# Optimization experiments

Hardware: AMD Instinct MI355X
Metric: run time of the kernel (lower is better)

The kernel has to match this reference:

```python
import jax, jax.numpy as jnp
import numpy as np

NEG = -1e30          # stand-in for -inf that is safe in fp arithmetic
EPS = 1e-7           # keras.backend.epsilon()

B, T, C, L = 64, 1024, 128, 256
BLANK = C - 1        # keras ctc_batch_cost uses last class as blank


def setup_inputs() -> dict:
    key = jax.random.key(0)
    k1, k2, k3 = jax.random.split(key, 3)
    # ctc_batch_cost expects softmax probabilities, not logits
    y_pred = jax.nn.softmax(jax.random.normal(k1, (B, T, C), dtype=jnp.float32), axis=-1)
    y_true = jax.random.randint(k2, (B, L), 0, C - 1).astype(jnp.int32)  # labels exclude blank
    input_length = jnp.full((B, 1), T, dtype=jnp.int32)
    label_length = jax.random.randint(k3, (B, 1), 1, L + 1).astype(jnp.int32)
    return {"y_true": y_true, "y_pred": y_pred,
            "input_length": input_length, "label_length": label_length}


def _logsumexp3(a, b, c):
    m = jnp.maximum(a, jnp.maximum(b, c))
    return m + jnp.log(jnp.exp(a - m) + jnp.exp(b - m) + jnp.exp(c - m))


def _ctc_loss(y_pred, y_true, input_length, label_length):
    log_probs = jnp.log(y_pred + EPS)                       # [B,T,C]
    S = 2 * L + 1
    # extended label sequence: blank, l0, blank, l1, ..., blank
    ext = jnp.full((B, S), BLANK, dtype=jnp.int32).at[:, 1::2].set(y_true)
    lab_len = label_length[:, 0]                            # [B]
    s_idx = jnp.arange(S)
    valid_s = s_idx[None, :] < (2 * lab_len + 1)[:, None]   # [B,S]
    # skip (s-2 -> s) allowed only for non-blank, non-repeated symbols
    skip_ok = jnp.concatenate(
        [jnp.zeros((B, 2), bool),
         (ext[:, 2:] != BLANK) & (ext[:, 2:] != ext[:, :-2])], axis=1)
    # gather per-extended-position log-probs: [B,T,S]
    lp_ext = jnp.take_along_axis(log_probs, jnp.broadcast_to(ext[:, None, :], (B, T, S)), axis=2)

    alpha0 = jnp.full((B, S), NEG, dtype=log_probs.dtype)
    alpha0 = alpha0.at[:, 0].set(lp_ext[:, 0, 0])
    alpha0 = alpha0.at[:, 1].set(jnp.where(lab_len > 0, lp_ext[:, 0, 1], NEG))
    alpha0 = jnp.where(valid_s, alpha0, NEG)

    def step(alpha, inp):
        lp_t, t = inp                                       # lp_t: [B,S]
        shift1 = jnp.pad(alpha[:, :-1], ((0, 0), (1, 0)), constant_values=NEG)
        shift2 = jnp.pad(alpha[:, :-2], ((0, 0), (2, 0)), constant_values=NEG)
        shift2 = jnp.where(skip_ok, shift2, NEG)
        new = _logsumexp3(alpha, shift1, shift2) + lp_t
        new = jnp.where(valid_s, new, NEG)
        # freeze alpha past each sample's input_length
        new = jnp.where(t < input_length, new, alpha)
        return new, None

    lp_tmaj = jnp.swapaxes(lp_ext, 0, 1)                    # [T,B,S]
    alpha, _ = jax.lax.scan(step, alpha0, (lp_tmaj[1:], jnp.arange(1, T)))

    end_blank = jnp.take_along_axis(alpha, (2 * lab_len)[:, None], axis=1)[:, 0]
    end_label = jnp.take_along_axis(alpha, jnp.maximum(2 * lab_len - 1, 0)[:, None], axis=1)[:, 0]
    end_label = jnp.where(lab_len > 0, end_label, NEG)
    loss = -jnp.logaddexp(end_blank, end_label)             # [B]
    return loss[:, None]                                    # (batch, 1) like ctc_batch_cost


def reference(y_true, y_pred, input_length, label_length):
    return _ctc_loss(y_pred, y_true, input_length, label_length)
```

## Files before the change

kernel.cpp:

```cpp
#include <hip/hip_runtime.h>


#define Bc 64
#define Tc 1024
#define Cc 128
#define Lc 256
#define Sc 513
#define BLANKc 127
#define CHUNK 32
#define NW 4
#define PADS 64
#define WSSTRIDE 1028

constexpr float EPSF = 1e-7f;

#define DPPMAXI(x, ctrl) max(x, __builtin_amdgcn_update_dpp( \
    0, x, ctrl, 0xf, 0xf, true))

__device__ __forceinline__ double dpp_wave_shr1_f64(double x) {
    union { double d; int i[2]; } u, r;
    u.d = x;
    r.i[0] = __builtin_amdgcn_update_dpp(0, u.i[0], 0x138, 0xf, 0xf, true);
    r.i[1] = __builtin_amdgcn_update_dpp(0, u.i[1], 0x138, 0xf, 0xf, true);
    return r.d;
}
__device__ __forceinline__ double dpp_wave_shl1_f64(double x) {
    union { double d; int i[2]; } u, r;
    u.d = x;
    r.i[0] = __builtin_amdgcn_update_dpp(0, u.i[0], 0x130, 0xf, 0xf, true);
    r.i[1] = __builtin_amdgcn_update_dpp(0, u.i[1], 0x130, 0xf, 0xf, true);
    return r.d;
}

__global__ __launch_bounds__(256) void ctc_fb_kernel(
    const int* __restrict__ y_true,
    const float* __restrict__ y_pred,
    const int* __restrict__ label_length,
    double* __restrict__ ws)
{
    const int bb = blockIdx.x;
    const int b = bb >> 1;
    const bool isF = !(bb & 1);
    const int tid = (int)threadIdx.x;
    const int wl = tid >> 6;
    const int lane = tid & 63;

    __shared__ float bufs[3][CHUNK * Cc];
    __shared__ double ash[Sc];
    __shared__ int em[NW];

    const int lab_len = label_length[b];
    const float* yp = y_pred + (size_t)b * Tc * Cc;
    const int* lab = y_true + b * Lc;
    double* wsb = ws + (size_t)b * WSSTRIDE;

    const int start = isF ? ((wl == 0) ? 0 : (128 * wl - PADS)) : (128 * wl);
    const int own_s = 128 * wl;
    const int own_e = (wl == NW - 1) ? Sc : (128 * (wl + 1));
    const int s0 = start + 4 * lane;

    const int li0 = s0 >> 1;
    const int li0c = min(li0, Lc - 1);
    const int li1c = min(li0 + 1, Lc - 1);
    const int li2c = min(li0 + 2, Lc - 1);
    const int ca = lab[li0c], cb = lab[li1c], cc = lab[li2c];
    const double sm_a = (li0 > 0 && ca != BLANKc && ca != lab[li0c - 1]) ? 1.0 : 0.0;
    const double sm_b = (cb != BLANKc && cb != ca) ? 1.0 : 0.0;
    const double sm_c = (cc != BLANKc && cc != cb) ? 1.0 : 0.0;

    const int S2 = 2 * lab_len + 1;
    const bool ow0 = (s0     >= own_s) && (s0     < own_e);
    const bool ow1 = (s0 + 1 >= own_s) && (s0 + 1 < own_e);
    const bool ow2 = (s0 + 2 >= own_s) && (s0 + 2 < own_e);
    const bool ow3 = (s0 + 3 >= own_s) && (s0 + 3 < own_e);
    const int om0 = (ow0 && s0     < S2) ? -1 : 0;
    const int om1 = (ow1 && s0 + 1 < S2) ? -1 : 0;
    const int om2 = (ow2 && s0 + 2 < S2) ? -1 : 0;
    const int om3 = (ow3 && s0 + 3 < S2) ? -1 : 0;

    auto stage = [&](int c, float* dst) {
        const float* g = yp + (size_t)c * (CHUNK * Cc) + lane * 4;
        #pragma unroll
        for (int q = 0; q < 4; ++q) {
            const int i = wl * 4 + q;
            __builtin_amdgcn_global_load_lds(
                (const __attribute__((address_space(1))) void*)(g + i * 256),
                (__attribute__((address_space(3))) void*)(dst + i * 256),
                16, 0, 0);
        }
    };

    if (isF) {
        double a0 = 0, a1 = 0, a2 = 0, a3 = 0, n3 = 0;
        int tote = 0;
        double Eb, Ea, Ec;
        double Ob, Oa, Oc;
        float sl[4][6];

        auto gpair = [&](const float* rowp, float* s) {
            s[0] = rowp[BLANKc]; s[1] = rowp[BLANKc + Cc];
            s[2] = rowp[ca];     s[3] = rowp[ca + Cc];
            s[4] = rowp[cb];     s[5] = rowp[cb + Cc];
        };
        auto expandE = [&](const float* s) {
            Eb = (double)(s[0] + EPSF); Ea = (double)(s[2] + EPSF);
            Ec = (double)(s[4] + EPSF);
        };
        auto expandO = [&](const float* s) {
            Ob = (double)(s[1] + EPSF); Oa = (double)(s[3] + EPSF);
            Oc = (double)(s[5] + EPSF);
        };
        auto stepE = [&]() {
            const double t3 = __fma_rn(sm_b, a1, a3 + a2);
            const double t2 = a2 + a1;
            const double t1 = __fma_rn(sm_a, n3, a1 + a0);
            const double t0 = a0 + n3;
            a3 = t3 * Ec;
            n3 = dpp_wave_shr1_f64(a3);
            a2 = t2 * Eb; a1 = t1 * Ea; a0 = t0 * Eb;
        };
        auto stepO = [&]() {
            const double t3 = __fma_rn(sm_b, a1, a3 + a2);
            const double t2 = a2 + a1;
            const double t1 = __fma_rn(sm_a, n3, a1 + a0);
            const double t0 = a0 + n3;
            a3 = t3 * Oc;
            n3 = dpp_wave_shr1_f64(a3);
            a2 = t2 * Ob; a1 = t1 * Oa; a0 = t0 * Ob;
        };
        auto syncex = [&](int sk) {
            int e =        om0 & (__double2hiint(a0) >> 20);
            e = max(e, om1 & (__double2hiint(a1) >> 20));
            e = max(e, om2 & (__double2hiint(a2) >> 20));
            e = max(e, om3 & (__double2hiint(a3) >> 20));
            e = DPPMAXI(e, 0x111); e = DPPMAXI(e, 0x112);
            e = DPPMAXI(e, 0x114); e = DPPMAXI(e, 0x118);
            e = DPPMAXI(e, 0x142); e = DPPMAXI(e, 0x143);
            if (lane == 63) em[wl] = e;
            if (ow0) ash[s0]     = a0;
            if (ow1) ash[s0 + 1] = a1;
            if (ow2) ash[s0 + 2] = a2;
            if (ow3) ash[s0 + 3] = a3;
            __syncthreads();
            const int eg = max(max(em[0], em[1]), max(em[2], em[3]));
            const int sexp = min(max(2046 - eg, 1), 2045);
            const double sc = __hiloint2double(sexp << 20, 0);
            tote += 1023 - sexp;
            if (wl > 0 && lane < (PADS / 4)) {
                a0 = ash[s0];     a1 = ash[s0 + 1];
                a2 = ash[s0 + 2]; a3 = ash[s0 + 3];
            }
            a0 *= sc; a1 *= sc; a2 *= sc; a3 *= sc;
            n3 = dpp_wave_shr1_f64(a3);
            __syncthreads();
            if (sk <= 15) stage(sk, bufs[sk % 3]);
        };

        stage(0, bufs[0]); stage(1, bufs[1]); stage(2, bufs[2]);
        __syncthreads();

        if (wl == 0 && lane == 0) {
            a0 = (double)(bufs[0][BLANKc] + EPSF);
            if (lab_len > 0) a1 = (double)(bufs[0][ca] + EPSF);
        }
        gpair(bufs[0] + 2 * Cc, sl[1]);
        gpair(bufs[0] + 4 * Cc, sl[2]);
        gpair(bufs[0] + 6 * Cc, sl[3]);
        {
            const float* r1 = bufs[0] + 1 * Cc;
            Ob = (double)(r1[BLANKc] + EPSF);
            Oa = (double)(r1[ca] + EPSF);
            Oc = (double)(r1[cb] + EPSF);
        }
        expandE(sl[1]);

        stepO();
        expandO(sl[1]);

        {
            const float* rb  = bufs[0];
            const float* rbn = bufs[1];
            #pragma unroll
            for (int qi = 1; qi < 16; ++qi) {
                const int rr = 2 * qi;
                const float* nxt = (rr + 6 < CHUNK) ? (rb + (rr + 6) * Cc)
                                                    : (rbn + (rr + 6 - CHUNK) * Cc);
                gpair(nxt, sl[(qi + 3) & 3]);
                stepE();
                expandE(sl[(qi + 1) & 3]);
                stepO();
                expandO(sl[(qi + 1) & 3]);
            }
        }
        for (int k = 1; k < 16; ++k) {
            syncex(k + 2);
            const float* rb  = bufs[k % 3];
            const float* rbn = bufs[(k + 1) % 3];
            #pragma unroll
            for (int qi = 0; qi < 16; ++qi) {
                const int rr = 2 * qi;
                const float* nxt = (rr + 6 < CHUNK) ? (rb + (rr + 6) * Cc)
                                                    : (rbn + (rr + 6 - CHUNK) * Cc);
                gpair(nxt, sl[(qi + 3) & 3]);
                stepE();
                expandE(sl[(qi + 1) & 3]);
                stepO();
                expandO(sl[(qi + 1) & 3]);
            }
        }
        if (ow0) wsb[s0]     = a0;
        if (ow1) wsb[s0 + 1] = a1;
        if (ow2) wsb[s0 + 2] = a2;
        if (ow3) wsb[s0 + 3] = a3;
        if (tid == 0) wsb[513] = (double)tote;
    } else {
        double b0 = 0, b1 = 0, b2 = 0, b3 = 0, n0 = 0, n1 = 0;
        int tote = 0;
        double Eb, Ea, Ec, Ed;
        double Ob, Oa, Oc, Od;
        float sl[4][8];

        auto gpair = [&](const float* rowp, float* s) {
            s[0] = rowp[BLANKc]; s[1] = rowp[BLANKc + Cc];
            s[2] = rowp[ca];     s[3] = rowp[ca + Cc];
            s[4] = rowp[cb];     s[5] = rowp[cb + Cc];
            s[6] = rowp[cc];     s[7] = rowp[cc + Cc];
        };
        auto expandE = [&](const float* s) {
            Eb = (double)(s[0] + EPSF); Ea = (double)(s[2] + EPSF);
            Ec = (double)(s[4] + EPSF); Ed = (double)(s[6] + EPSF);
        };
        auto expandO = [&](const float* s) {
            Ob = (double)(s[1] + EPSF); Oa = (double)(s[3] + EPSF);
            Oc = (double)(s[5] + EPSF); Od = (double)(s[7] + EPSF);
        };
        auto stepBE = [&]() {
            const double x1 = Ea * b1, x2 = Eb * b2, x3 = Ec * b3, z = Ed * n1;
            const double r0 = __fma_rn(Eb, b0, x1);
            const double r1 = __fma_rn(sm_b, x3, x1 + x2);
            const double r2 = x2 + x3;
            const double r3 = __fma_rn(sm_c, z, __fma_rn(Eb, n0, x3));
            b0 = r0; b1 = r1; b2 = r2; b3 = r3;
            n0 = dpp_wave_shl1_f64(b0);
            n1 = dpp_wave_shl1_f64(b1);
        };
        auto stepBO = [&]() {
            const double x1 = Oa * b1, x2 = Ob * b2, x3 = Oc * b3, z = Od * n1;
            const double r0 = __fma_rn(Ob, b0, x1);
            const double r1 = __fma_rn(sm_b, x3, x1 + x2);
            const double r2 = x2 + x3;
            const double r3 = __fma_rn(sm_c, z, __fma_rn(Ob, n0, x3));
            b0 = r0; b1 = r1; b2 = r2; b3 = r3;
            n0 = dpp_wave_shl1_f64(b0);
            n1 = dpp_wave_shl1_f64(b1);
        };
        auto syncex = [&](int sk) {
            int e =        om0 & (__double2hiint(b0) >> 20);
            e = max(e, om1 & (__double2hiint(b1) >> 20));
            e = max(e, om2 & (__double2hiint(b2) >> 20));
            e = max(e, om3 & (__double2hiint(b3) >> 20));
            e = DPPMAXI(e, 0x111); e = DPPMAXI(e, 0x112);
            e = DPPMAXI(e, 0x114); e = DPPMAXI(e, 0x118);
            e = DPPMAXI(e, 0x142); e = DPPMAXI(e, 0x143);
            if (lane == 63) em[wl] = e;
            if (ow0) ash[s0]     = b0;
            if (ow1) ash[s0 + 1] = b1;
            if (ow2) ash[s0 + 2] = b2;
            if (ow3) ash[s0 + 3] = b3;
            __syncthreads();
            const int eg = max(max(em[0], em[1]), max(em[2], em[3]));
            const int sexp = min(max(2046 - eg, 1), 2045);
            const double sc = __hiloint2double(sexp << 20, 0);
            tote += 1023 - sexp;
            if (s0     >= own_e) b0 = (s0     < Sc) ? ash[s0]     : 0.0;
            if (s0 + 1 >= own_e) b1 = (s0 + 1 < Sc) ? ash[s0 + 1] : 0.0;
            if (s0 + 2 >= own_e) b2 = (s0 + 2 < Sc) ? ash[s0 + 2] : 0.0;
            if (s0 + 3 >= own_e) b3 = (s0 + 3 < Sc) ? ash[s0 + 3] : 0.0;
            b0 *= sc; b1 *= sc; b2 *= sc; b3 *= sc;
            n0 = dpp_wave_shl1_f64(b0);
            n1 = dpp_wave_shl1_f64(b1);
            __syncthreads();
            if (sk >= 16) stage(sk, bufs[(31 - sk) % 3]);
        };

        stage(31, bufs[0]); stage(30, bufs[1]); stage(29, bufs[2]);
        __syncthreads();

        {
            const int e0 = 2 * lab_len;
            const int e1 = (lab_len > 0) ? (2 * lab_len - 1) : e0;
            b0 = (s0     == e0 || s0     == e1) ? 1.0 : 0.0;
            b1 = (s0 + 1 == e0 || s0 + 1 == e1) ? 1.0 : 0.0;
            b2 = (s0 + 2 == e0 || s0 + 2 == e1) ? 1.0 : 0.0;
            b3 = (s0 + 3 == e0 || s0 + 3 == e1) ? 1.0 : 0.0;
            n0 = dpp_wave_shl1_f64(b0);
            n1 = dpp_wave_shl1_f64(b1);
        }
        gpair(bufs[0] + 30 * Cc, sl[3]);
        gpair(bufs[0] + 28 * Cc, sl[2]);
        gpair(bufs[0] + 26 * Cc, sl[1]);
        expandO(sl[3]);
        expandE(sl[3]);

        {
            const float* rb  = bufs[0];
            const float* rbn = bufs[1];
            #pragma unroll
            for (int j = 0; j < 16; ++j) {
                const int q = 15 - j;
                const int rr = 2 * q;
                const float* nxt = (rr - 6 >= 0) ? (rb + (rr - 6) * Cc)
                                                 : (rbn + (rr - 6 + CHUNK) * Cc);
                gpair(nxt, sl[(q + 1) & 3]);
                stepBO();
                expandO(sl[(q - 1) & 3]);
                stepBE();
                expandE(sl[(q - 1) & 3]);
            }
        }
        for (int c = 30; c >= 16; --c) {
            syncex(c - 2);
            const float* rb  = bufs[(31 - c) % 3];
            const float* rbn = bufs[(32 - c) % 3];
            #pragma unroll
            for (int j = 0; j < 16; ++j) {
                const int q = 15 - j;
                const int rr = 2 * q;
                const float* nxt = (rr - 6 >= 0) ? (rb + (rr - 6) * Cc)
                                                 : (rbn + (rr - 6 + CHUNK) * Cc);
                gpair(nxt, sl[(q + 1) & 3]);
                stepBO();
                expandO(sl[(q - 1) & 3]);
                stepBE();
                expandE(sl[(q - 1) & 3]);
            }
        }
        if (ow0) wsb[514 + s0]     = b0;
        if (ow1) wsb[514 + s0 + 1] = b1;
        if (ow2) wsb[514 + s0 + 2] = b2;
        if (ow3) wsb[514 + s0 + 3] = b3;
        if (tid == 0) wsb[1027] = (double)tote;
    }
}

__global__ __launch_bounds__(64) void ctc_combine(
    const int* __restrict__ label_length,
    const double* __restrict__ ws,
    float* __restrict__ out)
{
    const int b = blockIdx.x;
    const int lane = (int)threadIdx.x;
    const int lab_len = label_length[b];
    const int S2 = 2 * lab_len + 1;
    const double* wf = ws + (size_t)b * WSSTRIDE;
    const double* wb = wf + 514;

    int eP = 0;
    for (int s = lane; s < S2; s += 64) {
        const int ea = (__double2hiint(wf[s]) >> 20) & 0x7ff;
        const int eb = (__double2hiint(wb[s]) >> 20) & 0x7ff;
        if (ea && eb) eP = max(eP, ea + eb);
    }
    #pragma unroll
    for (int m = 1; m < 64; m <<= 1) eP = max(eP, __shfl_xor(eP, m));
    const int sh = 2046 - eP;
    int k1 = sh / 2;
    int k2 = sh - k1;
    k1 = min(max(k1, -1022), 1023);
    k2 = min(max(k2, -1022), 1023);
    const double scA = __hiloint2double((1023 + k1) << 20, 0);
    const double scB = __hiloint2double((1023 + k2) << 20, 0);
    double dot = 0.0;
    for (int s = lane; s < S2; s += 64)
        dot += (wf[s] * scA) * (wb[s] * scB);
    #pragma unroll
    for (int m = 1; m < 64; m <<= 1) dot += __shfl_xor(dot, m);
    if (lane == 0) {
        const double lt = wf[513] + wb[513] - (double)k1 - (double)k2;
        out[b] = (float)(-(log(dot) + lt * 0.6931471805599453));
    }
}

extern "C" void kernel_launch(void* const* d_in, const int* in_sizes, int n_in,
                              void* d_out, int out_size, void* d_ws, size_t ws_size,
                              hipStream_t stream) {
    const int*   y_true       = (const int*)d_in[0];
    const float* y_pred       = (const float*)d_in[1];
    const int*   label_length = (const int*)d_in[3];
    float* out = (float*)d_out;
    double* ws = (double*)d_ws;

    ctc_fb_kernel<<<2 * Bc, NW * 64, 0, stream>>>(y_true, y_pred,
                                                  label_length, ws);
    ctc_combine<<<Bc, 64, 0, stream>>>(label_length, ws, out);
}
```

Measured before the change: 117.2 us.

## Split CTC forward/backward across 8 waves with 2 states per lane

Each block goes from 4 waves holding 4 extended-label states per lane to 8 waves holding 2 states per lane. Ownership ranges and the 64-position forward halo are redefined so each wave computes 128 positions and owns 64. This shortens the serial dependent FP64 work per time step in each lane. In exchange, every chunk sync barrier and exponent max-reduction now spans 8 waves, more redundant halo work is done, and the staging loads are spread over more waves.

```diff
diff --git a/kernel.cpp b/kernel.cpp
--- a/kernel.cpp
+++ b/kernel.cpp
@@ -8,8 +8,7 @@
 #define Sc 513
 #define BLANKc 127
 #define CHUNK 32
-#define NW 4
-#define PADS 64
+#define NW 8
 #define WSSTRIDE 1028
 
 constexpr float EPSF = 1e-7f;
@@ -32,7 +31,7 @@
     return r.d;
 }
 
-__global__ __launch_bounds__(256) void ctc_fb_kernel(
+__global__ __launch_bounds__(512) void ctc_fb_kernel(
     const int* __restrict__ y_true,
     const float* __restrict__ y_pred,
     const int* __restrict__ label_length,
@@ -54,35 +53,30 @@
     const int* lab = y_true + b * Lc;
     double* wsb = ws + (size_t)b * WSSTRIDE;
 
-    const int start = isF ? ((wl == 0) ? 0 : (128 * wl - PADS)) : (128 * wl);
-    const int own_s = 128 * wl;
-    const int own_e = (wl == NW - 1) ? Sc : (128 * (wl + 1));
-    const int s0 = start + 4 * lane;
+    const int start = 64 * wl;
+    const int s0 = start + 2 * lane;
+    const int own_s = isF ? ((wl == 0) ? 0 : (start + 64)) : start;
+    const int own_e = isF ? min(start + 128, Sc)
+                          : ((wl == NW - 1) ? Sc : (start + 64));
 
     const int li0 = s0 >> 1;
     const int li0c = min(li0, Lc - 1);
     const int li1c = min(li0 + 1, Lc - 1);
-    const int li2c = min(li0 + 2, Lc - 1);
-    const int ca = lab[li0c], cb = lab[li1c], cc = lab[li2c];
+    const int ca = lab[li0c], cb = lab[li1c];
     const double sm_a = (li0 > 0 && ca != BLANKc && ca != lab[li0c - 1]) ? 1.0 : 0.0;
     const double sm_b = (cb != BLANKc && cb != ca) ? 1.0 : 0.0;
-    const double sm_c = (cc != BLANKc && cc != cb) ? 1.0 : 0.0;
 
     const int S2 = 2 * lab_len + 1;
     const bool ow0 = (s0     >= own_s) && (s0     < own_e);
     const bool ow1 = (s0 + 1 >= own_s) && (s0 + 1 < own_e);
-    const bool ow2 = (s0 + 2 >= own_s) && (s0 + 2 < own_e);
-    const bool ow3 = (s0 + 3 >= own_s) && (s0 + 3 < own_e);
     const int om0 = (ow0 && s0     < S2) ? -1 : 0;
     const int om1 = (ow1 && s0 + 1 < S2) ? -1 : 0;
-    const int om2 = (ow2 && s0 + 2 < S2) ? -1 : 0;
-    const int om3 = (ow3 && s0 + 3 < S2) ? -1 : 0;
 
     auto stage = [&](int c, float* dst) {
         const float* g = yp + (size_t)c * (CHUNK * Cc) + lane * 4;
         #pragma unroll
-        for (int q = 0; q < 4; ++q) {
-            const int i = wl * 4 + q;
+        for (int q = 0; q < 2; ++q) {
+            const int i = wl * 2 + q;
             __builtin_amdgcn_global_load_lds(
                 (const __attribute__((address_space(1))) void*)(g + i * 256),
                 (__attribute__((address_space(3))) void*)(dst + i * 256),
@@ -91,67 +85,57 @@
     };
 
     if (isF) {
-        double a0 = 0, a1 = 0, a2 = 0, a3 = 0, n3 = 0;
+        double a0 = 0, a1 = 0, n1 = 0;
         int tote = 0;
-        double Eb, Ea, Ec;
-        double Ob, Oa, Oc;
-        float sl[4][6];
+        double Eb, Ea;
+        double Ob, Oa;
+        float sl[4][4];
 
         auto gpair = [&](const float* rowp, float* s) {
             s[0] = rowp[BLANKc]; s[1] = rowp[BLANKc + Cc];
             s[2] = rowp[ca];     s[3] = rowp[ca + Cc];
-            s[4] = rowp[cb];     s[5] = rowp[cb + Cc];
         };
         auto expandE = [&](const float* s) {
             Eb = (double)(s[0] + EPSF); Ea = (double)(s[2] + EPSF);
-            Ec = (double)(s[4] + EPSF);
         };
         auto expandO = [&](const float* s) {
             Ob = (double)(s[1] + EPSF); Oa = (double)(s[3] + EPSF);
-            Oc = (double)(s[5] + EPSF);
         };
         auto stepE = [&]() {
-            const double t3 = __fma_rn(sm_b, a1, a3 + a2);
-            const double t2 = a2 + a1;
-            const double t1 = __fma_rn(sm_a, n3, a1 + a0);
-            const double t0 = a0 + n3;
-            a3 = t3 * Ec;
-            n3 = dpp_wave_shr1_f64(a3);
-            a2 = t2 * Eb; a1 = t1 * Ea; a0 = t0 * Eb;
+            const double t1 = __fma_rn(sm_a, n1, a1 + a0);
+            const double t0 = a0 + n1;
+            a1 = t1 * Ea;
+            n1 = dpp_wave_shr1_f64(a1);
+            a0 = t0 * Eb;
         };
         auto stepO = [&]() {
-            const double t3 = __fma_rn(sm_b, a1, a3 + a2);
-            const double t2 = a2 + a1;
-            const double t1 = __fma_rn(sm_a, n3, a1 + a0);
-            const double t0 = a0 + n3;
-            a3 = t3 * Oc;
-            n3 = dpp_wave_shr1_f64(a3);
-            a2 = t2 * Ob; a1 = t1 * Oa; a0 = t0 * Ob;
+            const double t1 = __fma_rn(sm_a, n1, a1 + a0);
+            const double t0 = a0 + n1;
+            a1 = t1 * Oa;
+            n1 = dpp_wave_shr1_f64(a1);
+            a0 = t0 * Ob;
         };
         auto syncex = [&](int sk) {
             int e =        om0 & (__double2hiint(a0) >> 20);
             e = max(e, om1 & (__double2hiint(a1) >> 20));
-            e = max(e, om2 & (__double2hiint(a2) >> 20));
-            e = max(e, om3 & (__double2hiint(a3) >> 20));
             e = DPPMAXI(e, 0x111); e = DPPMAXI(e, 0x112);
             e = DPPMAXI(e, 0x114); e = DPPMAXI(e, 0x118);
             e = DPPMAXI(e, 0x142); e = DPPMAXI(e, 0x143);
             if (lane == 63) em[wl] = e;
             if (ow0) ash[s0]     = a0;
             if (ow1) ash[s0 + 1] = a1;
-            if (ow2) ash[s0 + 2] = a2;
-            if (ow3) ash[s0 + 3] = a3;
             __syncthreads();
-            const int eg = max(max(em[0], em[1]), max(em[2], em[3]));
+            int eg = em[0];
+            #pragma unroll
+            for (int w = 1; w < NW; ++w) eg = max(eg, em[w]);
             const int sexp = min(max(2046 - eg, 1), 2045);
             const double sc = __hiloint2double(sexp << 20, 0);
             tote += 1023 - sexp;
-            if (wl > 0 && lane < (PADS / 4)) {
-                a0 = ash[s0];     a1 = ash[s0 + 1];
-                a2 = ash[s0 + 2]; a3 = ash[s0 + 3];
-            }
-            a0 *= sc; a1 *= sc; a2 *= sc; a3 *= sc;
-            n3 = dpp_wave_shr1_f64(a3);
+            if (wl > 0 && lane < 32) {
+                a0 = ash[s0]; a1 = ash[s0 + 1];
+            }
+            a0 *= sc; a1 *= sc;
+            n1 = dpp_wave_shr1_f64(a1);
             __syncthreads();
             if (sk <= 15) stage(sk, bufs[sk % 3]);
         };
@@ -170,7 +154,6 @@
             const float* r1 = bufs[0] + 1 * Cc;
             Ob = (double)(r1[BLANKc] + EPSF);
             Oa = (double)(r1[ca] + EPSF);
-            Oc = (double)(r1[cb] + EPSF);
         }
         expandE(sl[1]);
 
@@ -210,73 +193,62 @@
         }
         if (ow0) wsb[s0]     = a0;
         if (ow1) wsb[s0 + 1] = a1;
-        if (ow2) wsb[s0 + 2] = a2;
-        if (ow3) wsb[s0 + 3] = a3;
         if (tid == 0) wsb[513] = (double)tote;
     } else {
-        double b0 = 0, b1 = 0, b2 = 0, b3 = 0, n0 = 0, n1 = 0;
+        double b0 = 0, b1 = 0, n0 = 0, n1 = 0;
         int tote = 0;
-        double Eb, Ea, Ec, Ed;
-        double Ob, Oa, Oc, Od;
-        float sl[4][8];
+        double Eb, Ea, Ec;
+        double Ob, Oa, Oc;
+        float sl[4][6];
 
         auto gpair = [&](const float* rowp, float* s) {
             s[0] = rowp[BLANKc]; s[1] = rowp[BLANKc + Cc];
             s[2] = rowp[ca];     s[3] = rowp[ca + Cc];
             s[4] = rowp[cb];     s[5] = rowp[cb + Cc];
-            s[6] = rowp[cc];     s[7] = rowp[cc + Cc];
         };
         auto expandE = [&](const float* s) {
             Eb = (double)(s[0] + EPSF); Ea = (double)(s[2] + EPSF);
-            Ec = (double)(s[4] + EPSF); Ed = (double)(s[6] + EPSF);
+            Ec = (double)(s[4] + EPSF);
         };
         auto expandO = [&](const float* s) {
             Ob = (double)(s[1] + EPSF); Oa = (double)(s[3] + EPSF);
-            Oc = (double)(s[5] + EPSF); Od = (double)(s[7] + EPSF);
+            Oc = (double)(s[5] + EPSF);
         };
         auto stepBE = [&]() {
-            const double x1 = Ea * b1, x2 = Eb * b2, x3 = Ec * b3, z = Ed * n1;
+            const double x1 = Ea * b1, x2 = Eb * n0, x3 = Ec * n1;
             const double r0 = __fma_rn(Eb, b0, x1);
             const double r1 = __fma_rn(sm_b, x3, x1 + x2);
-            const double r2 = x2 + x3;
-            const double r3 = __fma_rn(sm_c, z, __fma_rn(Eb, n0, x3));
-            b0 = r0; b1 = r1; b2 = r2; b3 = r3;
+            b0 = r0; b1 = r1;
             n0 = dpp_wave_shl1_f64(b0);
             n1 = dpp_wave_shl1_f64(b1);
         };
         auto stepBO = [&]() {
-            const double x1 = Oa * b1, x2 = Ob * b2, x3 = Oc * b3, z = Od * n1;
+            const double x1 = Oa * b1, x2 = Ob * n0, x3 = Oc * n1;
             const double r0 = __fma_rn(Ob, b0, x1);
             const double r1 = __fma_rn(sm_b, x3, x1 + x2);
-            const double r2 = x2 + x3;
-            const double r3 = __fma_rn(sm_c, z, __fma_rn(Ob, n0, x3));
-            b0 = r0; b1 = r1; b2 = r2; b3 = r3;
+            b0 = r0; b1 = r1;
             n0 = dpp_wave_shl1_f64(b0);
             n1 = dpp_wave_shl1_f64(b1);
         };
         auto syncex = [&](int sk) {
             int e =        om0 & (__double2hiint(b0) >> 20);
             e = max(e, om1 & (__double2hiint(b1) >> 20));
-            e = max(e, om2 & (__double2hiint(b2) >> 20));
-            e = max(e, om3 & (__double2hiint(b3) >> 20));
             e = DPPMAXI(e, 0x111); e = DPPMAXI(e, 0x112);
             e = DPPMAXI(e, 0x114); e = DPPMAXI(e, 0x118);
             e = DPPMAXI(e, 0x142); e = DPPMAXI(e, 0x143);
             if (lane == 63) em[wl] = e;
             if (ow0) ash[s0]     = b0;
             if (ow1) ash[s0 + 1] = b1;
-            if (ow2) ash[s0 + 2] = b2;
-            if (ow3) ash[s0 + 3] = b3;
             __syncthreads();
-            const int eg = max(max(em[0], em[1]), max(em[2], em[3]));
+            int eg = em[0];
+            #pragma unroll
+            for (int w = 1; w < NW; ++w) eg = max(eg, em[w]);
             const int sexp = min(max(2046 - eg, 1), 2045);
             const double sc = __hiloint2double(sexp << 20, 0);
             tote += 1023 - sexp;
             if (s0     >= own_e) b0 = (s0     < Sc) ? ash[s0]     : 0.0;
             if (s0 + 1 >= own_e) b1 = (s0 + 1 < Sc) ? ash[s0 + 1] : 0.0;
-            if (s0 + 2 >= own_e) b2 = (s0 + 2 < Sc) ? ash[s0 + 2] : 0.0;
-            if (s0 + 3 >= own_e) b3 = (s0 + 3 < Sc) ? ash[s0 + 3] : 0.0;
-            b0 *= sc; b1 *= sc; b2 *= sc; b3 *= sc;
+            b0 *= sc; b1 *= sc;
             n0 = dpp_wave_shl1_f64(b0);
             n1 = dpp_wave_shl1_f64(b1);
             __syncthreads();
@@ -291,8 +263,6 @@
             const int e1 = (lab_len > 0) ? (2 * lab_len - 1) : e0;
             b0 = (s0     == e0 || s0     == e1) ? 1.0 : 0.0;
             b1 = (s0 + 1 == e0 || s0 + 1 == e1) ? 1.0 : 0.0;
-            b2 = (s0 + 2 == e0 || s0 + 2 == e1) ? 1.0 : 0.0;
-            b3 = (s0 + 3 == e0 || s0 + 3 == e1) ? 1.0 : 0.0;
             n0 = dpp_wave_shl1_f64(b0);
             n1 = dpp_wave_shl1_f64(b1);
         }
@@ -337,8 +307,6 @@
         }
         if (ow0) wsb[514 + s0]     = b0;
         if (ow1) wsb[514 + s0 + 1] = b1;
-        if (ow2) wsb[514 + s0 + 2] = b2;
-        if (ow3) wsb[514 + s0 + 3] = b3;
         if (tid == 0) wsb[1027] = (double)tote;
     }
 }
```

New measurement: 117.7 us. No clear change (+0.4%).

## Bulk-load per-chunk probability columns into registers, fetch blank column from global

Applied to the files above, without the earlier changes.

Replaces the rolling 4-slot software pipeline of per-row LDS reads with a bulk load of all 32 rows of the needed columns into register arrays at the start of each chunk. The blank column is read straight from global memory rather than LDS, and the backward pass's fourth class column is obtained by a DPP lane shift of the neighbour's value instead of a separate LDS read. Launch bounds are set to one block per CU so the larger register arrays fit. The change cuts LDS traffic and address arithmetic inside the recurrence, but it adds register pressure and puts global-memory latency at the start of each chunk.

```diff
diff --git a/kernel.cpp b/kernel.cpp
--- a/kernel.cpp
+++ b/kernel.cpp
@@ -31,8 +31,14 @@
     r.i[1] = __builtin_amdgcn_update_dpp(0, u.i[1], 0x130, 0xf, 0xf, true);
     return r.d;
 }
-
-__global__ __launch_bounds__(256) void ctc_fb_kernel(
+__device__ __forceinline__ float dpp_wave_shl1_f32(float x) {
+    union { float f; int i; } u, r;
+    u.f = x;
+    r.i = __builtin_amdgcn_update_dpp(0, u.i, 0x130, 0xf, 0xf, true);
+    return r.f;
+}
+
+__global__ __launch_bounds__(256, 1) void ctc_fb_kernel(
     const int* __restrict__ y_true,
     const float* __restrict__ y_pred,
     const int* __restrict__ label_length,
@@ -90,26 +96,25 @@
         }
     };
 
+    float cB[CHUNK];
+    float cA[CHUNK];
+    float cC[CHUNK];
+
+    auto loadcols = [&](int c, const float* rb) {
+        const float* gB = yp + (size_t)c * (CHUNK * Cc) + BLANKc;
+        #pragma unroll
+        for (int t = 0; t < CHUNK; ++t) {
+            cA[t] = rb[t * Cc + ca];
+            cC[t] = rb[t * Cc + cb];
+            cB[t] = gB[t * Cc];
+        }
+    };
+
     if (isF) {
         double a0 = 0, a1 = 0, a2 = 0, a3 = 0, n3 = 0;
         int tote = 0;
-        double Eb, Ea, Ec;
-        double Ob, Oa, Oc;
-        float sl[4][6];
-
-        auto gpair = [&](const float* rowp, float* s) {
-            s[0] = rowp[BLANKc]; s[1] = rowp[BLANKc + Cc];
-            s[2] = rowp[ca];     s[3] = rowp[ca + Cc];
-            s[4] = rowp[cb];     s[5] = rowp[cb + Cc];
-        };
-        auto expandE = [&](const float* s) {
-            Eb = (double)(s[0] + EPSF); Ea = (double)(s[2] + EPSF);
-            Ec = (double)(s[4] + EPSF);
-        };
-        auto expandO = [&](const float* s) {
-            Ob = (double)(s[1] + EPSF); Oa = (double)(s[3] + EPSF);
-            Oc = (double)(s[5] + EPSF);
-        };
+        double Eb, Ea, Ec, Ob, Oa, Oc;
+
         auto stepE = [&]() {
             const double t3 = __fma_rn(sm_b, a1, a3 + a2);
             const double t2 = a2 + a1;
@@ -127,6 +132,16 @@
             a3 = t3 * Oc;
             n3 = dpp_wave_shr1_f64(a3);
             a2 = t2 * Ob; a1 = t1 * Oa; a0 = t0 * Ob;
+        };
+        auto dopair = [&](int r) {
+            Eb = (double)(cB[r] + EPSF);
+            Ea = (double)(cA[r] + EPSF);
+            Ec = (double)(cC[r] + EPSF);
+            stepE();
+            Ob = (double)(cB[r + 1] + EPSF);
+            Oa = (double)(cA[r + 1] + EPSF);
+            Oc = (double)(cC[r + 1] + EPSF);
+            stepO();
         };
         auto syncex = [&](int sk) {
             int e =        om0 & (__double2hiint(a0) >> 20);
@@ -159,54 +174,23 @@
         stage(0, bufs[0]); stage(1, bufs[1]); stage(2, bufs[2]);
         __syncthreads();
 
+        loadcols(0, bufs[0]);
         if (wl == 0 && lane == 0) {
-            a0 = (double)(bufs[0][BLANKc] + EPSF);
-            if (lab_len > 0) a1 = (double)(bufs[0][ca] + EPSF);
-        }
-        gpair(bufs[0] + 2 * Cc, sl[1]);
-        gpair(bufs[0] + 4 * Cc, sl[2]);
-        gpair(bufs[0] + 6 * Cc, sl[3]);
-        {
-            const float* r1 = bufs[0] + 1 * Cc;
-            Ob = (double)(r1[BLANKc] + EPSF);
-            Oa = (double)(r1[ca] + EPSF);
-            Oc = (double)(r1[cb] + EPSF);
-        }
-        expandE(sl[1]);
-
+            a0 = (double)(cB[0] + EPSF);
+            if (lab_len > 0) a1 = (double)(cA[0] + EPSF);
+        }
+        Ob = (double)(cB[1] + EPSF);
+        Oa = (double)(cA[1] + EPSF);
+        Oc = (double)(cC[1] + EPSF);
         stepO();
-        expandO(sl[1]);
-
-        {
-            const float* rb  = bufs[0];
-            const float* rbn = bufs[1];
-            #pragma unroll
-            for (int qi = 1; qi < 16; ++qi) {
-                const int rr = 2 * qi;
-                const float* nxt = (rr + 6 < CHUNK) ? (rb + (rr + 6) * Cc)
-                                                    : (rbn + (rr + 6 - CHUNK) * Cc);
-                gpair(nxt, sl[(qi + 3) & 3]);
-                stepE();
-                expandE(sl[(qi + 1) & 3]);
-                stepO();
-                expandO(sl[(qi + 1) & 3]);
-            }
-        }
+        #pragma unroll
+        for (int p = 1; p < 16; ++p) dopair(2 * p);
+
         for (int k = 1; k < 16; ++k) {
             syncex(k + 2);
-            const float* rb  = bufs[k % 3];
-            const float* rbn = bufs[(k + 1) % 3];
+            loadcols(k, bufs[k % 3]);
             #pragma unroll
-            for (int qi = 0; qi < 16; ++qi) {
-                const int rr = 2 * qi;
-                const float* nxt = (rr + 6 < CHUNK) ? (rb + (rr + 6) * Cc)
-                                                    : (rbn + (rr + 6 - CHUNK) * Cc);
-                gpair(nxt, sl[(qi + 3) & 3]);
-                stepE();
-                expandE(sl[(qi + 1) & 3]);
-                stepO();
-                expandO(sl[(qi + 1) & 3]);
-            }
+            for (int p = 0; p < 16; ++p) dopair(2 * p);
         }
         if (ow0) wsb[s0]     = a0;
         if (ow1) wsb[s0 + 1] = a1;
@@ -216,24 +200,8 @@
     } else {
         double b0 = 0, b1 = 0, b2 = 0, b3 = 0, n0 = 0, n1 = 0;
         int tote = 0;
-        double Eb, Ea, Ec, Ed;
-        double Ob, Oa, Oc, Od;
-        float sl[4][8];
-
-        auto gpair = [&](const float* rowp, float* s) {
-            s[0] = rowp[BLANKc]; s[1] = rowp[BLANKc + Cc];
-            s[2] = rowp[ca];     s[3] = rowp[ca + Cc];
-            s[4] = rowp[cb];     s[5] = rowp[cb + Cc];
-            s[6] = rowp[cc];     s[7] = rowp[cc + Cc];
-        };
-        auto expandE = [&](const float* s) {
-            Eb = (double)(s[0] + EPSF); Ea = (double)(s[2] + EPSF);
-            Ec = (double)(s[4] + EPSF); Ed = (double)(s[6] + EPSF);
-        };
-        auto expandO = [&](const float* s) {
-            Ob = (double)(s[1] + EPSF); Oa = (double)(s[3] + EPSF);
-            Oc = (double)(s[5] + EPSF); Od = (double)(s[7] + EPSF);
-        };
+        double Eb, Ea, Ec, Ed, Ob, Oa, Oc, Od;
+
         auto stepBE = [&]() {
             const double x1 = Ea * b1, x2 = Eb * b2, x3 = Ec * b3, z = Ed * n1;
             const double r0 = __fma_rn(Eb, b0, x1);
@@ -253,6 +221,18 @@
             b0 = r0; b1 = r1; b2 = r2; b3 = r3;
             n0 = dpp_wave_shl1_f64(b0);
             n1 = dpp_wave_shl1_f64(b1);
+        };
+        auto dopairB = [&](int r) {
+            Ob = (double)(cB[r + 1] + EPSF);
+            Oa = (double)(cA[r + 1] + EPSF);
+            Oc = (double)(cC[r + 1] + EPSF);
+            Od = (double)(dpp_wave_shl1_f32(cA[r + 1]) + EPSF);
+            stepBO();
+            Eb = (double)(cB[r] + EPSF);
+            Ea = (double)(cA[r] + EPSF);
+            Ec = (double)(cC[r] + EPSF);
+            Ed = (double)(dpp_wave_shl1_f32(cA[r]) + EPSF);
+            stepBE();
         };
         auto syncex = [&](int sk) {
             int e =        om0 & (__double2hiint(b0) >> 20);
@@ -296,44 +276,15 @@
             n0 = dpp_wave_shl1_f64(b0);
             n1 = dpp_wave_shl1_f64(b1);
         }
-        gpair(bufs[0] + 30 * Cc, sl[3]);
-        gpair(bufs[0] + 28 * Cc, sl[2]);
-        gpair(bufs[0] + 26 * Cc, sl[1]);
-        expandO(sl[3]);
-        expandE(sl[3]);
-
-        {
-            const float* rb  = bufs[0];
-            const float* rbn = bufs[1];
-            #pragma unroll
-            for (int j = 0; j < 16; ++j) {
-                const int q = 15 - j;
-                const int rr = 2 * q;
-                const float* nxt = (rr - 6 >= 0) ? (rb + (rr - 6) * Cc)
-                                                 : (rbn + (rr - 6 + CHUNK) * Cc);
-                gpair(nxt, sl[(q + 1) & 3]);
-                stepBO();
-                expandO(sl[(q - 1) & 3]);
-                stepBE();
-                expandE(sl[(q - 1) & 3]);
-            }
-        }
+        loadcols(31, bufs[0]);
+        #pragma unroll
+        for (int p = 15; p >= 0; --p) dopairB(2 * p);
+
         for (int c = 30; c >= 16; --c) {
             syncex(c - 2);
-            const float* rb  = bufs[(31 - c) % 3];
-            const float* rbn = bufs[(32 - c) % 3];
+            loadcols(c, bufs[(31 - c) % 3]);
             #pragma unroll
-            for (int j = 0; j < 16; ++j) {
-                const int q = 15 - j;
-                const int rr = 2 * q;
-                const float* nxt = (rr - 6 >= 0) ? (rb + (rr - 6) * Cc)
-                                                 : (rbn + (rr - 6 + CHUNK) * Cc);
-                gpair(nxt, sl[(q + 1) & 3]);
-                stepBO();
-                expandO(sl[(q - 1) & 3]);
-                stepBE();
-                expandE(sl[(q - 1) & 3]);
-            }
+            for (int p = 15; p >= 0; --p) dopairB(2 * p);
         }
         if (ow0) wsb[514 + s0]     = b0;
         if (ow1) wsb[514 + s0 + 1] = b1;
```

Measured after the change: 119.8 us. 1.02x slower.

## Load blank probs from global, deepen LDS prefetch ring, derive backward cc via DPP

Applied to the files above, without the earlier changes.

Blank-class probabilities, which are the same address for every lane, are now read straight from global memory instead of LDS, lowering LDS traffic and bank pressure. The software prefetch of per-row values grows from a 4-deep to an 8-deep register ring, looking six row-pairs ahead instead of three. The backward pass drops its fourth per-lane LDS gather and gets that value by shifting the neighbour lane's label probability with a DPP lane shift. Launch bounds add a minimum of one block per SIMD, so the compiler can use more registers. The costs are higher register pressure and global loads that may not be hidden across chunk boundaries.

```diff
diff --git a/kernel.cpp b/kernel.cpp
--- a/kernel.cpp
+++ b/kernel.cpp
@@ -31,8 +31,14 @@
     r.i[1] = __builtin_amdgcn_update_dpp(0, u.i[1], 0x130, 0xf, 0xf, true);
     return r.d;
 }
-
-__global__ __launch_bounds__(256) void ctc_fb_kernel(
+__device__ __forceinline__ float dpp_wave_shl1_f32(float x) {
+    union { float f; int i; } u, r;
+    u.f = x;
+    r.i = __builtin_amdgcn_update_dpp(0, u.i, 0x130, 0xf, 0xf, true);
+    return r.f;
+}
+
+__global__ __launch_bounds__(256, 1) void ctc_fb_kernel(
     const int* __restrict__ y_true,
     const float* __restrict__ y_pred,
     const int* __restrict__ label_length,
@@ -90,18 +96,20 @@
         }
     };
 
+    float sl[8][6];
+
+    auto gpair = [&](const float* rowp, const float* growp, float* s) {
+        s[0] = growp[0];
+        s[1] = growp[Cc];
+        s[2] = rowp[ca]; s[3] = rowp[ca + Cc];
+        s[4] = rowp[cb]; s[5] = rowp[cb + Cc];
+    };
+
     if (isF) {
         double a0 = 0, a1 = 0, a2 = 0, a3 = 0, n3 = 0;
         int tote = 0;
-        double Eb, Ea, Ec;
-        double Ob, Oa, Oc;
-        float sl[4][6];
-
-        auto gpair = [&](const float* rowp, float* s) {
-            s[0] = rowp[BLANKc]; s[1] = rowp[BLANKc + Cc];
-            s[2] = rowp[ca];     s[3] = rowp[ca + Cc];
-            s[4] = rowp[cb];     s[5] = rowp[cb + Cc];
-        };
+        double Eb, Ea, Ec, Ob, Oa, Oc;
+
         auto expandE = [&](const float* s) {
             Eb = (double)(s[0] + EPSF); Ea = (double)(s[2] + EPSF);
             Ec = (double)(s[4] + EPSF);
@@ -163,9 +171,10 @@
             a0 = (double)(bufs[0][BLANKc] + EPSF);
             if (lab_len > 0) a1 = (double)(bufs[0][ca] + EPSF);
         }
-        gpair(bufs[0] + 2 * Cc, sl[1]);
-        gpair(bufs[0] + 4 * Cc, sl[2]);
-        gpair(bufs[0] + 6 * Cc, sl[3]);
+        #pragma unroll
+        for (int pp = 1; pp <= 6; ++pp)
+            gpair(bufs[0] + 2 * pp * Cc,
+                  yp + (size_t)(2 * pp) * Cc + BLANKc, sl[pp]);
         {
             const float* r1 = bufs[0] + 1 * Cc;
             Ob = (double)(r1[BLANKc] + EPSF);
@@ -180,32 +189,34 @@
         {
             const float* rb  = bufs[0];
             const float* rbn = bufs[1];
+            const float* gB  = yp + BLANKc;
             #pragma unroll
             for (int qi = 1; qi < 16; ++qi) {
-                const int rr = 2 * qi;
-                const float* nxt = (rr + 6 < CHUNK) ? (rb + (rr + 6) * Cc)
-                                                    : (rbn + (rr + 6 - CHUNK) * Cc);
-                gpair(nxt, sl[(qi + 3) & 3]);
+                const int ra = 2 * qi + 12;
+                const float* nxt = (ra < CHUNK) ? (rb + ra * Cc)
+                                                : (rbn + (ra - CHUNK) * Cc);
+                gpair(nxt, gB + (size_t)ra * Cc, sl[(qi + 6) & 7]);
                 stepE();
-                expandE(sl[(qi + 1) & 3]);
+                expandE(sl[(qi + 1) & 7]);
                 stepO();
-                expandO(sl[(qi + 1) & 3]);
+                expandO(sl[(qi + 1) & 7]);
             }
         }
         for (int k = 1; k < 16; ++k) {
             syncex(k + 2);
             const float* rb  = bufs[k % 3];
             const float* rbn = bufs[(k + 1) % 3];
+            const float* gB  = yp + (size_t)k * (CHUNK * Cc) + BLANKc;
             #pragma unroll
             for (int qi = 0; qi < 16; ++qi) {
-                const int rr = 2 * qi;
-                const float* nxt = (rr + 6 < CHUNK) ? (rb + (rr + 6) * Cc)
-                                                    : (rbn + (rr + 6 - CHUNK) * Cc);
-                gpair(nxt, sl[(qi + 3) & 3]);
+                const int ra = 2 * qi + 12;
+                const float* nxt = (ra < CHUNK) ? (rb + ra * Cc)
+                                                : (rbn + (ra - CHUNK) * Cc);
+                gpair(nxt, gB + (size_t)ra * Cc, sl[(qi + 6) & 7]);
                 stepE();
-                expandE(sl[(qi + 1) & 3]);
+                expandE(sl[(qi + 1) & 7]);
                 stepO();
-                expandO(sl[(qi + 1) & 3]);
+                expandO(sl[(qi + 1) & 7]);
             }
         }
         if (ow0) wsb[s0]     = a0;
@@ -216,23 +227,17 @@
     } else {
         double b0 = 0, b1 = 0, b2 = 0, b3 = 0, n0 = 0, n1 = 0;
         int tote = 0;
-        double Eb, Ea, Ec, Ed;
-        double Ob, Oa, Oc, Od;
-        float sl[4][8];
-
-        auto gpair = [&](const float* rowp, float* s) {
-            s[0] = rowp[BLANKc]; s[1] = rowp[BLANKc + Cc];
-            s[2] = rowp[ca];     s[3] = rowp[ca + Cc];
-            s[4] = rowp[cb];     s[5] = rowp[cb + Cc];
-            s[6] = rowp[cc];     s[7] = rowp[cc + Cc];
-        };
-        auto expandE = [&](const float* s) {
+        double Eb, Ea, Ec, Ed, Ob, Oa, Oc, Od;
+
+        auto expandEB = [&](const float* s) {
             Eb = (double)(s[0] + EPSF); Ea = (double)(s[2] + EPSF);
-            Ec = (double)(s[4] + EPSF); Ed = (double)(s[6] + EPSF);
-        };
-        auto expandO = [&](const float* s) {
+            Ec = (double)(s[4] + EPSF);
+            Ed = (double)(dpp_wave_shl1_f32(s[2]) + EPSF);
+        };
+        auto expandOB = [&](const float* s) {
             Ob = (double)(s[1] + EPSF); Oa = (double)(s[3] + EPSF);
-            Oc = (double)(s[5] + EPSF); Od = (double)(s[7] + EPSF);
+            Oc = (double)(s[5] + EPSF);
+            Od = (double)(dpp_wave_shl1_f32(s[3]) + EPSF);
         };
         auto stepBE = [&]() {
             const double x1 = Ea * b1, x2 = Eb * b2, x3 = Ec * b3, z = Ed * n1;
@@ -296,43 +301,49 @@
             n0 = dpp_wave_shl1_f64(b0);
             n1 = dpp_wave_shl1_f64(b1);
         }
-        gpair(bufs[0] + 30 * Cc, sl[3]);
-        gpair(bufs[0] + 28 * Cc, sl[2]);
-        gpair(bufs[0] + 26 * Cc, sl[1]);
-        expandO(sl[3]);
-        expandE(sl[3]);
+        #pragma unroll
+        for (int pp = 0; pp < 6; ++pp) {
+            const int pr = 15 - pp;
+            gpair(bufs[0] + 2 * pr * Cc,
+                  yp + (size_t)(31 * CHUNK + 2 * pr) * Cc + BLANKc,
+                  sl[pr & 7]);
+        }
+        expandOB(sl[7]);
+        expandEB(sl[7]);
 
         {
             const float* rb  = bufs[0];
             const float* rbn = bufs[1];
+            const float* gB  = yp + (size_t)(31 * CHUNK) * Cc + BLANKc;
             #pragma unroll
             for (int j = 0; j < 16; ++j) {
                 const int q = 15 - j;
-                const int rr = 2 * q;
-                const float* nxt = (rr - 6 >= 0) ? (rb + (rr - 6) * Cc)
-                                                 : (rbn + (rr - 6 + CHUNK) * Cc);
-                gpair(nxt, sl[(q + 1) & 3]);
+                const int ra = 2 * q - 12;
+                const float* nxt = (ra >= 0) ? (rb + ra * Cc)
+                                             : (rbn + (ra + CHUNK) * Cc);
+                gpair(nxt, gB + (ptrdiff_t)ra * Cc, sl[(q + 2) & 7]);
                 stepBO();
-                expandO(sl[(q - 1) & 3]);
+                expandOB(sl[(q - 1) & 7]);
                 stepBE();
-                expandE(sl[(q - 1) & 3]);
+                expandEB(sl[(q - 1) & 7]);
             }
         }
         for (int c = 30; c >= 16; --c) {
             syncex(c - 2);
             const float* rb  = bufs[(31 - c) % 3];
             const float* rbn = bufs[(32 - c) % 3];
+            const float* gB  = yp + (size_t)c * (CHUNK * Cc) + BLANKc;
             #pragma unroll
             for (int j = 0; j < 16; ++j) {
                 const int q = 15 - j;
-                const int rr = 2 * q;
-                const float* nxt = (rr - 6 >= 0) ? (rb + (rr - 6) * Cc)
-                                                 : (rbn + (rr - 6 + CHUNK) * Cc);
-                gpair(nxt, sl[(q + 1) & 3]);
+                const int ra = 2 * q - 12;
+                const float* nxt = (ra >= 0) ? (rb + ra * Cc)
+                                             : (rbn + (ra + CHUNK) * Cc);
+                gpair(nxt, gB + (ptrdiff_t)ra * Cc, sl[(q + 2) & 7]);
                 stepBO();
-                expandO(sl[(q - 1) & 3]);
+                expandOB(sl[(q - 1) & 7]);
                 stepBE();
-                expandE(sl[(q - 1) & 3]);
+                expandEB(sl[(q - 1) & 7]);
             }
         }
         if (ow0) wsb[514 + s0]     = b0;
```

After: 121.4 us. 1.04x slower.
